# Optimization experiments

Measured on AMD Instinct MI355X. Metric: run time of the kernel, lower is better.

Reference implementation:

```python
import jax, jax.numpy as jnp
import numpy as np


def setup_inputs() -> dict:
    key = jax.random.key(0)
    k1, k2, k3 = jax.random.split(key, 3)
    x = jax.random.normal(k1, (32, 256, 64, 64), dtype=jnp.float32)
    w = jax.random.normal(k2, (1, 1, 7, 7), dtype=jnp.float32) * (1.0 / 7.0)
    b = jax.random.normal(k3, (1,), dtype=jnp.float32) * 0.1
    return {"x": x, "w": w, "b": b}


def reference(x, w, b):
    # channel-wise mean and max pooling, keepdim -> [B,1,H,W]
    pooled = jnp.mean(x, axis=1, keepdims=True) + jnp.max(x, axis=1, keepdims=True)
    # 7x7 conv, 1->1 channel, SAME padding (pad=3)
    attn = jax.lax.conv_general_dilated(
        pooled, w,
        window_strides=(1, 1),
        padding=((3, 3), (3, 3)),
        dimension_numbers=("NCHW", "OIHW", "NCHW"),
    ) + b[None, :, None, None]
    attn = jax.nn.sigmoid(attn)
    return x * attn  # broadcast over channels
```

## Files before the change

### kernel.cpp

```cpp
#include <hip/hip_runtime.h>
#include <math.h>

#define BATCH 32
#define CH    256
#define HH    64
#define WW    64
#define HW    (HH * WW)
#define NPIX  (BATCH * HW)
#define NTOT  ((size_t)BATCH * CH * HW)

__global__ __launch_bounds__(256) void sa_pool_kernel(
    const float* __restrict__ x, float* __restrict__ pooled) {
    int idx = blockIdx.x * blockDim.x + threadIdx.x;
    if (idx >= NPIX) return;
    int b  = idx >> 12;
    int hw = idx & 4095;
    const float* p = x + (size_t)b * CH * HW + hw;
    float s = 0.0f;
    float m = -INFINITY;
#pragma unroll 8
    for (int c = 0; c < CH; ++c) {
        float v = p[(size_t)c * HW];
        s += v;
        m = fmaxf(m, v);
    }
    pooled[idx] = s * (1.0f / (float)CH) + m;
}

__global__ __launch_bounds__(256) void sa_conv_kernel(
    const float* __restrict__ pooled, const float* __restrict__ wgt,
    const float* __restrict__ bias, float* __restrict__ attn) {
    int idx = blockIdx.x * blockDim.x + threadIdx.x;
    if (idx >= NPIX) return;
    int b  = idx >> 12;
    int hw = idx & 4095;
    int h  = hw >> 6;
    int w  = hw & 63;
    const float* pb = pooled + b * HW;
    float acc = bias[0];
#pragma unroll
    for (int kh = 0; kh < 7; ++kh) {
        int hh2 = h + kh - 3;
        if (hh2 < 0 || hh2 >= HH) continue;
#pragma unroll
        for (int kw = 0; kw < 7; ++kw) {
            int ww2 = w + kw - 3;
            if (ww2 < 0 || ww2 >= WW) continue;
            acc += pb[hh2 * WW + ww2] * wgt[kh * 7 + kw];
        }
    }
    attn[idx] = 1.0f / (1.0f + __expf(-acc));
}

__global__ __launch_bounds__(256) void sa_mul_kernel(
    const float* __restrict__ x, const float* __restrict__ attn,
    float* __restrict__ out) {
    size_t i = ((size_t)blockIdx.x * blockDim.x + threadIdx.x) * 4;
    if (i >= NTOT) return;
    size_t bc = i >> 12;
    int hw    = (int)(i & 4095);
    int b     = (int)(bc >> 8);
    float4 xv = *reinterpret_cast<const float4*>(x + i);
    float4 av = *reinterpret_cast<const float4*>(attn + (size_t)b * HW + hw);
    float4 o;
    o.x = xv.x * av.x;
    o.y = xv.y * av.y;
    o.z = xv.z * av.z;
    o.w = xv.w * av.w;
    *reinterpret_cast<float4*>(out + i) = o;
}

extern "C" void kernel_launch(void* const* d_in, const int* in_sizes, int n_in,
                              void* d_out, int out_size, void* d_ws, size_t ws_size,
                              hipStream_t stream) {
    const float* x    = (const float*)d_in[0];
    const float* wgt  = (const float*)d_in[1];
    const float* bias = (const float*)d_in[2];
    float* out = (float*)d_out;

    float* pooled = (float*)d_ws;
    float* attn   = pooled + NPIX;

    {
        dim3 block(256);
        dim3 grid((NPIX + 255) / 256);
        sa_pool_kernel<<<grid, block, 0, stream>>>(x, pooled);
    }
    {
        dim3 block(256);
        dim3 grid((NPIX + 255) / 256);
        sa_conv_kernel<<<grid, block, 0, stream>>>(pooled, wgt, bias, attn);
    }
    {
        dim3 block(256);
        dim3 grid((unsigned)((NTOT / 4 + 255) / 256));
        sa_mul_kernel<<<grid, block, 0, stream>>>(x, attn, out);
    }
}
```

Before: 77.79 us.

## Split channel pooling into chunked float4 partials plus combine kernel; nontemporal output stores

The channel reduction is split across 8 channel chunks with float4 loads per thread, which gives more parallel threads and wider memory accesses. A new combine kernel merges the partial sums and maxes into the pooled map. The multiply kernel now writes its output with nontemporal stores so the result does not pollute the cache. The cost is one extra launch and extra workspace traffic for the partial buffers.

```diff
diff --git a/kernel.cpp b/kernel.cpp
--- a/kernel.cpp
+++ b/kernel.cpp
@@ -7,24 +7,56 @@
 #define WW    64
 #define HW    (HH * WW)
 #define NPIX  (BATCH * HW)
+#define PG    (NPIX / 4)
 #define NTOT  ((size_t)BATCH * CH * HW)
+#define NCHUNK 8
+#define CCHUNK (CH / NCHUNK)
 
-__global__ __launch_bounds__(256) void sa_pool_kernel(
-    const float* __restrict__ x, float* __restrict__ pooled) {
-    int idx = blockIdx.x * blockDim.x + threadIdx.x;
-    if (idx >= NPIX) return;
-    int b  = idx >> 12;
-    int hw = idx & 4095;
-    const float* p = x + (size_t)b * CH * HW + hw;
-    float s = 0.0f;
-    float m = -INFINITY;
+typedef float floatx4 __attribute__((ext_vector_type(4)));
+
+__global__ __launch_bounds__(256) void sa_pool_partial_kernel(
+    const float* __restrict__ x,
+    float4* __restrict__ pSum, float4* __restrict__ pMax) {
+    int t = blockIdx.x * blockDim.x + threadIdx.x;
+    int pg    = t & (PG - 1);
+    int chunk = t >> 15;
+    int b   = pg >> 10;
+    int hwg = pg & 1023;
+    const float4* p = reinterpret_cast<const float4*>(
+        x + (size_t)b * CH * HW + (size_t)chunk * CCHUNK * HW) + hwg;
+    float4 s = make_float4(0.f, 0.f, 0.f, 0.f);
+    float4 m = make_float4(-INFINITY, -INFINITY, -INFINITY, -INFINITY);
 #pragma unroll 8
-    for (int c = 0; c < CH; ++c) {
-        float v = p[(size_t)c * HW];
-        s += v;
-        m = fmaxf(m, v);
+    for (int c = 0; c < CCHUNK; ++c) {
+        float4 v = p[c * (HW / 4)];
+        s.x += v.x; s.y += v.y; s.z += v.z; s.w += v.w;
+        m.x = fmaxf(m.x, v.x); m.y = fmaxf(m.y, v.y);
+        m.z = fmaxf(m.z, v.z); m.w = fmaxf(m.w, v.w);
     }
-    pooled[idx] = s * (1.0f / (float)CH) + m;
+    pSum[chunk * PG + pg] = s;
+    pMax[chunk * PG + pg] = m;
+}
+
+__global__ __launch_bounds__(256) void sa_pool_combine_kernel(
+    const float4* __restrict__ pSum, const float4* __restrict__ pMax,
+    float4* __restrict__ pooled) {
+    int pg = blockIdx.x * blockDim.x + threadIdx.x;
+    if (pg >= PG) return;
+    float4 s = make_float4(0.f, 0.f, 0.f, 0.f);
+    float4 m = make_float4(-INFINITY, -INFINITY, -INFINITY, -INFINITY);
+#pragma unroll
+    for (int c = 0; c < NCHUNK; ++c) {
+        float4 sv = pSum[c * PG + pg];
+        float4 mv = pMax[c * PG + pg];
+        s.x += sv.x; s.y += sv.y; s.z += sv.z; s.w += sv.w;
+        m.x = fmaxf(m.x, mv.x); m.y = fmaxf(m.y, mv.y);
+        m.z = fmaxf(m.z, mv.z); m.w = fmaxf(m.w, mv.w);
+    }
+    const float inv = 1.0f / (float)CH;
+    float4 o;
+    o.x = s.x * inv + m.x; o.y = s.y * inv + m.y;
+    o.z = s.z * inv + m.z; o.w = s.w * inv + m.w;
+    pooled[pg] = o;
 }
 
 __global__ __launch_bounds__(256) void sa_conv_kernel(
@@ -62,12 +94,12 @@
     int b     = (int)(bc >> 8);
     float4 xv = *reinterpret_cast<const float4*>(x + i);
     float4 av = *reinterpret_cast<const float4*>(attn + (size_t)b * HW + hw);
-    float4 o;
+    floatx4 o;
     o.x = xv.x * av.x;
     o.y = xv.y * av.y;
     o.z = xv.z * av.z;
     o.w = xv.w * av.w;
-    *reinterpret_cast<float4*>(out + i) = o;
+    __builtin_nontemporal_store(o, reinterpret_cast<floatx4*>(out + i));
 }
 
 extern "C" void kernel_launch(void* const* d_in, const int* in_sizes, int n_in,
@@ -78,13 +110,21 @@
     const float* bias = (const float*)d_in[2];
     float* out = (float*)d_out;
 
-    float* pooled = (float*)d_ws;
-    float* attn   = pooled + NPIX;
+    float*  pooled = (float*)d_ws;
+    float*  attn   = pooled + NPIX;
+    float4* pSum   = reinterpret_cast<float4*>(attn + NPIX);
+    float4* pMax   = pSum + (size_t)NCHUNK * PG;
 
     {
         dim3 block(256);
-        dim3 grid((NPIX + 255) / 256);
-        sa_pool_kernel<<<grid, block, 0, stream>>>(x, pooled);
+        dim3 grid((PG * NCHUNK) / 256);
+        sa_pool_partial_kernel<<<grid, block, 0, stream>>>(x, pSum, pMax);
+    }
+    {
+        dim3 block(256);
+        dim3 grid((PG + 255) / 256);
+        sa_pool_combine_kernel<<<grid, block, 0, stream>>>(
+            pSum, pMax, reinterpret_cast<float4*>(pooled));
     }
     {
         dim3 block(256);
```

After: 78.64 us. No clear change (+1.1%).

## Split channel reduction across warps with float4 loads in pooling kernel

Applied to the files above, without the earlier changes.

Each pooling block now covers 128 pixels of one image. Its 8 thread groups each reduce 32 channels using float4 loads, and the partial sums and maxes are combined through shared memory. The old kernel had each thread loop serially over all 256 channels with scalar loads. The new layout gives more memory parallelism per thread and wider loads. In exchange it adds a shared-memory reduction step and a sync.

```diff
diff --git a/kernel.cpp b/kernel.cpp
--- a/kernel.cpp
+++ b/kernel.cpp
@@ -9,25 +9,56 @@
 #define NPIX  (BATCH * HW)
 #define NTOT  ((size_t)BATCH * CH * HW)
 
-__global__ __launch_bounds__(256) void sa_pool_kernel(
-    const float* __restrict__ x, float* __restrict__ pooled) {
-    int idx = blockIdx.x * blockDim.x + threadIdx.x;
-    if (idx >= NPIX) return;
-    int b  = idx >> 12;
-    int hw = idx & 4095;
-    const float* p = x + (size_t)b * CH * HW + hw;
-    float s = 0.0f;
-    float m = -INFINITY;
+#define PIX_PER_BLK 128
+#define GRP_PER_BLK 32
+#define NCHUNK 8
+#define CCHUNK 32
+#define NBLK  (NPIX / PIX_PER_BLK)
+
+__global__ __launch_bounds__(256) void sa_pool(
+    const float* __restrict__ x, float4* __restrict__ pooled4) {
+    __shared__ float4 sS[NCHUNK][GRP_PER_BLK];
+    __shared__ float4 sM[NCHUNK][GRP_PER_BLK];
+    int t = threadIdx.x;
+    int g = t & 31;
+    int c = t >> 5;
+    int img = blockIdx.x >> 5;
+    int seg = blockIdx.x & 31;
+    int pix0 = seg * PIX_PER_BLK;
+    const float* p = x + (size_t)img * CH * HW + (size_t)c * CCHUNK * HW
+                   + pix0 + g * 4;
+    float4 s = make_float4(0.f, 0.f, 0.f, 0.f);
+    float4 m = make_float4(-INFINITY, -INFINITY, -INFINITY, -INFINITY);
 #pragma unroll 8
-    for (int c = 0; c < CH; ++c) {
-        float v = p[(size_t)c * HW];
-        s += v;
-        m = fmaxf(m, v);
+    for (int i = 0; i < CCHUNK; ++i) {
+        float4 v = *reinterpret_cast<const float4*>(p + (size_t)i * HW);
+        s.x += v.x; s.y += v.y; s.z += v.z; s.w += v.w;
+        m.x = fmaxf(m.x, v.x); m.y = fmaxf(m.y, v.y);
+        m.z = fmaxf(m.z, v.z); m.w = fmaxf(m.w, v.w);
     }
-    pooled[idx] = s * (1.0f / (float)CH) + m;
+    sS[c][g] = s;
+    sM[c][g] = m;
+    __syncthreads();
+    if (t < GRP_PER_BLK) {
+        float4 as = sS[0][t];
+        float4 am = sM[0][t];
+#pragma unroll
+        for (int cc = 1; cc < NCHUNK; ++cc) {
+            float4 bs = sS[cc][t];
+            float4 bm = sM[cc][t];
+            as.x += bs.x; as.y += bs.y; as.z += bs.z; as.w += bs.w;
+            am.x = fmaxf(am.x, bm.x); am.y = fmaxf(am.y, bm.y);
+            am.z = fmaxf(am.z, bm.z); am.w = fmaxf(am.w, bm.w);
+        }
+        const float inv = 1.0f / (float)CH;
+        float4 o;
+        o.x = as.x * inv + am.x; o.y = as.y * inv + am.y;
+        o.z = as.z * inv + am.z; o.w = as.w * inv + am.w;
+        pooled4[(img * HW + pix0) / 4 + t] = o;
+    }
 }
 
-__global__ __launch_bounds__(256) void sa_conv_kernel(
+__global__ __launch_bounds__(256) void sa_conv(
     const float* __restrict__ pooled, const float* __restrict__ wgt,
     const float* __restrict__ bias, float* __restrict__ attn) {
     int idx = blockIdx.x * blockDim.x + threadIdx.x;
@@ -52,7 +83,7 @@
     attn[idx] = 1.0f / (1.0f + __expf(-acc));
 }
 
-__global__ __launch_bounds__(256) void sa_mul_kernel(
+__global__ __launch_bounds__(256) void sa_mul(
     const float* __restrict__ x, const float* __restrict__ attn,
     float* __restrict__ out) {
     size_t i = ((size_t)blockIdx.x * blockDim.x + threadIdx.x) * 4;
@@ -81,19 +112,10 @@
     float* pooled = (float*)d_ws;
     float* attn   = pooled + NPIX;
 
-    {
-        dim3 block(256);
-        dim3 grid((NPIX + 255) / 256);
-        sa_pool_kernel<<<grid, block, 0, stream>>>(x, pooled);
-    }
-    {
-        dim3 block(256);
-        dim3 grid((NPIX + 255) / 256);
-        sa_conv_kernel<<<grid, block, 0, stream>>>(pooled, wgt, bias, attn);
-    }
-    {
-        dim3 block(256);
-        dim3 grid((unsigned)((NTOT / 4 + 255) / 256));
-        sa_mul_kernel<<<grid, block, 0, stream>>>(x, attn, out);
-    }
+    sa_pool<<<dim3(NBLK), dim3(256), 0, stream>>>(
+        x, reinterpret_cast<float4*>(pooled));
+    sa_conv<<<dim3((NPIX + 255) / 256), dim3(256), 0, stream>>>(
+        pooled, wgt, bias, attn);
+    sa_mul<<<dim3((unsigned)((NTOT / 4 + 255) / 256)), dim3(256), 0, stream>>>(
+        x, attn, out);
 }
```

Result: faster. 74.60 us (-4.1%).
